# Kernel tuning notes

Hardware: AMD Instinct MI355X
Metric: run time of the kernel (lower is better)

## Reference

```python
import jax, jax.numpy as jnp
import numpy as np

V, E, H, B, S = 32000, 512, 1024, 128, 64
EPS = 0.05


def setup_inputs() -> dict:
    key = jax.random.key(0)
    ks = jax.random.split(key, 4)
    s = 0.02
    return {
        "emb": jax.random.normal(ks[0], (V, E), jnp.float32) * s,
        "w_ih": jax.random.normal(ks[1], (3 * H, E), jnp.float32) * s,
        "w_hh": jax.random.normal(ks[2], (3 * H, H), jnp.float32) * s,
        "b_ih": jnp.zeros((3 * H,), jnp.float32),
        "b_hh": jnp.zeros((3 * H,), jnp.float32),
        "w_dist": jax.random.normal(ks[3], (V, H), jnp.float32) * s,
        "b_dist": jnp.zeros((V,), jnp.float32),
    }


def reference(emb, w_ih, w_hh, b_ih, b_hh, w_dist, b_dist):
    base = jax.random.key(42)
    log_unif = -jnp.log(jnp.float32(V))  # log prob of uniform draw
    rows = jnp.arange(B)

    def step(carry, t):
        h, x = carry
        # PyTorch GRUCell math
        gx = x @ w_ih.T + b_ih            # [B, 3H]
        gh = h @ w_hh.T + b_hh            # [B, 3H]
        xr, xz, xn = jnp.split(gx, 3, axis=1)
        hr, hz, hn = jnp.split(gh, 3, axis=1)
        r = jax.nn.sigmoid(xr + hr)
        z = jax.nn.sigmoid(xz + hz)
        n = jnp.tanh(xn + r * hn)
        h_new = (1.0 - z) * n + z * h     # [B, H]

        dist = jax.nn.log_softmax(h_new @ w_dist.T + b_dist, axis=-1)  # [B, V]
        dist_sg = jax.lax.stop_gradient(dist)  # .detach() in torch

        k = jax.random.fold_in(base, t)
        k1, k2 = jax.random.split(k)
        # epsilon-exploration: replace whole row by uniform log-prob
        draw = jax.random.uniform(k1, (B,)) <= EPS
        dist_new = jnp.where(draw[:, None], log_unif, dist_sg)
        # Gumbel-max categorical sampling: argmax(dist_new - log(-log U))
        gumbel = -jnp.log(-jnp.log(jax.random.uniform(k2, (B, V))))
        sampled = jnp.argmax(dist_new + gumbel, axis=1)  # [B] int

        logprob = dist[rows, sampled]                                # [B]
        onp = jnp.clip(jnp.exp(dist_sg[rows, sampled]), 1e-8, 1.0)
        offp = jnp.clip(jnp.exp(dist_new[rows, sampled]), 1e-8, 1.0)
        correction = onp / offp
        prob_mean = jnp.mean(jnp.exp(dist_sg), axis=0)               # [V]

        x_next = emb[sampled]  # feed sampled token back in
        return (h_new, x_next), (sampled, correction, logprob, prob_mean)

    h0 = jnp.zeros((B, H), emb.dtype)
    x0 = jnp.broadcast_to(emb[0], (B, E))  # embedding of zero_input
    _, (samp, corr, lp, probs) = jax.lax.scan(step, (h0, x0), jnp.arange(S))
    # stack along time then transpose to [B, S] like torch.cat(..., 1)
    return samp.T, corr.T, lp.T, probs
```

## Files before the change

### kernel.cpp

```cpp
#include <hip/hip_runtime.h>
#include <cstdint>
#include <cmath>

#define V 32000
#define E 512
#define H 1024
#define B 128
#define S 64
#define NCHUNK 8
#define CHUNK 4000
#define PSTRIDE 250
#define BS (B*S)
#define NEG_HUGE (-3.0e38f)

typedef __attribute__((ext_vector_type(8))) short short8;
typedef __attribute__((ext_vector_type(4))) float f32x4;

#define TFR(x0, x1, r) { x0 += x1; x1 = ((x1) << (r)) | ((x1) >> (32 - (r))); x1 ^= x0; }

__host__ __device__ inline void tf2x32(uint32_t k0, uint32_t k1, uint32_t &x0, uint32_t &x1) {
  uint32_t ks2 = k0 ^ k1 ^ 0x1BD11BDAu;
  x0 += k0; x1 += k1;
  TFR(x0,x1,13) TFR(x0,x1,15) TFR(x0,x1,26) TFR(x0,x1,6)
  x0 += k1;  x1 += ks2 + 1u;
  TFR(x0,x1,17) TFR(x0,x1,29) TFR(x0,x1,16) TFR(x0,x1,24)
  x0 += ks2; x1 += k0 + 2u;
  TFR(x0,x1,13) TFR(x0,x1,15) TFR(x0,x1,26) TFR(x0,x1,6)
  x0 += k0;  x1 += k1 + 3u;
  TFR(x0,x1,17) TFR(x0,x1,29) TFR(x0,x1,16) TFR(x0,x1,24)
  x0 += k1;  x1 += ks2 + 4u;
  TFR(x0,x1,13) TFR(x0,x1,15) TFR(x0,x1,26) TFR(x0,x1,6)
  x0 += ks2; x1 += k0 + 5u;
}

__device__ __forceinline__ uint32_t tf_bits32(uint32_t ka, uint32_t kb, uint32_t idx) {
  uint32_t x0 = 0u, x1 = idx;
  tf2x32(ka, kb, x0, x1);
  return x0 ^ x1;
}

__device__ __forceinline__ float bits_to_unif(uint32_t b) {
  return __uint_as_float((b >> 9) | 0x3f800000u) - 1.0f;
}

__device__ __forceinline__ float sigmoidf_(float x) { return 1.0f / (1.0f + expf(-x)); }

__device__ __forceinline__ ushort f2bf(float f) {
  uint32_t u = __float_as_uint(f);
  uint32_t r = u + 0x7FFFu + ((u >> 16) & 1u);
  return (ushort)(r >> 16);
}
__device__ __forceinline__ float bf2f(ushort h) { return __uint_as_float(((uint32_t)h) << 16); }

__device__ __forceinline__ void gload16(const ushort* g, ushort* l) {
  __builtin_amdgcn_global_load_lds((const __attribute__((address_space(1))) void*)g,
                                   (__attribute__((address_space(3))) void*)l, 16, 0, 0);
}

template<int BM, int BN, int BK, int TM, int TN>
__device__ void gemm_tile(const float* __restrict__ A, const float* __restrict__ Wt,
                          const float* __restrict__ bias, float* __restrict__ C,
                          int N, int K, int mblk, int nblk)
{
  constexpr int WP = BN + 4;
  __shared__ __align__(16) float As[BK][BM];
  __shared__ __align__(16) float Ws[BK][WP];
  const int tid = threadIdx.x;
  constexpr int TX = BN / TN;
  constexpr int TY = BM / TM;
  static_assert(TX * TY == 256, "bad tiling");
  const int tx = tid % TX, ty = tid / TX;
  const int n0 = tx * TN, m0 = ty * TM;

  float acc[TM][TN];
#pragma unroll
  for (int i = 0; i < TM; ++i)
#pragma unroll
    for (int j = 0; j < TN; ++j) acc[i][j] = 0.0f;

  constexpr int NA = (BM * BK / 4) / 256;
  constexpr int NW = (BN * BK / 4) / 256;
  static_assert(NA >= 1 && NW >= 1, "tile too small");

  for (int k0 = 0; k0 < K; k0 += BK) {
    __syncthreads();
#pragma unroll
    for (int q = 0; q < NA; ++q) {
      int idx = q * 256 + tid;
      int m = idx / (BK / 4), c = idx % (BK / 4);
      float4 v = *(const float4*)&A[(size_t)(mblk + m) * K + k0 + 4 * c];
      As[4*c+0][m] = v.x; As[4*c+1][m] = v.y; As[4*c+2][m] = v.z; As[4*c+3][m] = v.w;
    }
#pragma unroll
    for (int q = 0; q < NW; ++q) {
      int idx = q * 256 + tid;
      int n = idx / (BK / 4), c = idx % (BK / 4);
      float4 v = *(const float4*)&Wt[(size_t)(nblk + n) * K + k0 + 4 * c];
      Ws[4*c+0][n] = v.x; Ws[4*c+1][n] = v.y; Ws[4*c+2][n] = v.z; Ws[4*c+3][n] = v.w;
    }
    __syncthreads();
#pragma unroll
    for (int k = 0; k < BK; ++k) {
      float a[TM], w[TN];
#pragma unroll
      for (int i = 0; i < TM; ++i) a[i] = As[k][m0 + i];
#pragma unroll
      for (int j = 0; j < TN; ++j) w[j] = Ws[k][n0 + j];
#pragma unroll
      for (int i = 0; i < TM; ++i)
#pragma unroll
        for (int j = 0; j < TN; ++j) acc[i][j] += a[i] * w[j];
    }
  }
#pragma unroll
  for (int i = 0; i < TM; ++i)
#pragma unroll
    for (int j = 0; j < TN; ++j)
      C[(size_t)(mblk + m0 + i) * N + nblk + n0 + j] = acc[i][j] + bias[nblk + n0 + j];
}

__global__ __launch_bounds__(256) void gemm_dist_k(const float* __restrict__ h,
    const float* __restrict__ w_dist, const float* __restrict__ b_dist,
    float* __restrict__ logits)
{
  gemm_tile<128, 64, 16, 8, 4>(h, w_dist, b_dist, logits, V, H, 0, blockIdx.x * 64);
}

__global__ __launch_bounds__(256) void gemm_gru_k(const float* __restrict__ x,
    const float* __restrict__ h, const float* __restrict__ w_ih, const float* __restrict__ w_hh,
    const float* __restrict__ b_ih, const float* __restrict__ b_hh,
    float* __restrict__ gx, float* __restrict__ gh)
{
  int b = blockIdx.x;
  if (b < 96) {
    int rb = b & 1, cb = b >> 1;
    gemm_tile<64, 64, 16, 4, 4>(x, w_ih, b_ih, gx, 3 * H, E, rb * 64, cb * 64);
  } else {
    b -= 96;
    int rb = b & 1, cb = b >> 1;
    gemm_tile<64, 64, 16, 4, 4>(h, w_hh, b_hh, gh, 3 * H, H, rb * 64, cb * 64);
  }
}

__global__ __launch_bounds__(256) void wsplit_k(const float* __restrict__ w,
    ushort* __restrict__ whi, ushort* __restrict__ wlo, int n4)
{
  int idx = blockIdx.x * 256 + threadIdx.x;
  if (idx >= n4) return;
  size_t i = (size_t)idx * 4;
  float4 v = *(const float4*)&w[i];
  ushort h0 = f2bf(v.x), h1 = f2bf(v.y), h2 = f2bf(v.z), h3 = f2bf(v.w);
  ushort l0 = f2bf(v.x - bf2f(h0)), l1 = f2bf(v.y - bf2f(h1));
  ushort l2 = f2bf(v.z - bf2f(h2)), l3 = f2bf(v.w - bf2f(h3));
  ushort4 hv = {h0, h1, h2, h3}, lv = {l0, l1, l2, l3};
  *(ushort4*)&whi[i] = hv;
  *(ushort4*)&wlo[i] = lv;
}

__global__ __launch_bounds__(256) void gru_gates_k(const float* __restrict__ gx,
    const float* __restrict__ gh, float* __restrict__ h,
    ushort* __restrict__ hhi, ushort* __restrict__ hlo)
{
  int idx = blockIdx.x * 256 + threadIdx.x;
  int b = idx >> 10, j = idx & 1023;
  const float* gxb = gx + (size_t)b * 3 * H;
  const float* ghb = gh + (size_t)b * 3 * H;
  float r = sigmoidf_(gxb[j] + ghb[j]);
  float z = sigmoidf_(gxb[H + j] + ghb[H + j]);
  float n = tanhf(gxb[2 * H + j] + r * ghb[2 * H + j]);
  float hn = (1.0f - z) * n + z * h[idx];
  h[idx] = hn;
  ushort hi = f2bf(hn);
  hhi[idx] = hi;
  hlo[idx] = f2bf(hn - bf2f(hi));
}

__global__ __launch_bounds__(512) void gemm_dist_mfma(const ushort* __restrict__ hhi,
    const ushort* __restrict__ hlo, const ushort* __restrict__ whi,
    const ushort* __restrict__ wlo, const float* __restrict__ b_dist,
    float* __restrict__ logits,
    float* __restrict__ pm, float* __restrict__ ps,
    float* __restrict__ pbest, int* __restrict__ pidx,
    uint32_t k1a, uint32_t k1b, uint32_t k2a, uint32_t k2b)
{
  __shared__ ushort Ah[2][128 * 32], Al[2][128 * 32], Wh[2][128 * 32], Wl[2][128 * 32];
  __shared__ float rm[2 * 128], rs[2 * 128], rb_[2 * 128];
  __shared__ int   ri[2 * 128];
  __shared__ uint32_t sdraw[128];
  const int tid = threadIdx.x;
  const int wave = tid >> 6, lane = tid & 63;
  const int wm = (wave & 3) * 32;
  const int wn = (wave >> 2) * 64;
  const int nblk = blockIdx.x * 128;
  const int l15 = lane & 15;
  const int q = lane >> 4;

  if (tid < 128)
    sdraw[tid] = (bits_to_unif(tf_bits32(k1a, k1b, (uint32_t)tid)) <= 0.05f) ? 1u : 0u;

  const int sr = tid >> 2;
  const int gq8 = ((tid & 3) ^ ((sr >> 1) & 3)) * 8;
  const size_t arow = (size_t)sr * 1024 + gq8;
  const size_t wrow = (size_t)(nblk + sr) * 1024 + gq8;
  const int wbase = wave * 512;

#define DIST_STAGE(bf, kk) {                                   \
    gload16(&hhi[arow + (kk)], &Ah[bf][wbase]);                \
    gload16(&hlo[arow + (kk)], &Al[bf][wbase]);                \
    gload16(&whi[wrow + (kk)], &Wh[bf][wbase]);                \
    gload16(&wlo[wrow + (kk)], &Wl[bf][wbase]);                \
  }

  f32x4 acc[2][4] = {};

  DIST_STAGE(0, 0);

  int buf = 0;
  for (int k0 = 0; k0 < 1024; k0 += 32, buf ^= 1) {
    const bool more = (k0 + 32 < 1024);
    if (more) {
      DIST_STAGE(buf ^ 1, k0 + 32);
      asm volatile("s_waitcnt vmcnt(4)" ::: "memory");
    } else {
      asm volatile("s_waitcnt vmcnt(0)" ::: "memory");
    }
    __builtin_amdgcn_sched_barrier(0);
    __builtin_amdgcn_s_barrier();
    __builtin_amdgcn_sched_barrier(0);

    short8 ah[2], al[2], wh[4], wl[4];
#pragma unroll
    for (int mt = 0; mt < 2; ++mt) {
      int row = wm + mt * 16 + l15;
      int off = row * 32 + ((q ^ ((row >> 1) & 3)) * 8);
      ah[mt] = *(const short8*)&Ah[buf][off];
      al[mt] = *(const short8*)&Al[buf][off];
    }
#pragma unroll
    for (int nt = 0; nt < 4; ++nt) {
      int row = wn + nt * 16 + l15;
      int off = row * 32 + ((q ^ ((row >> 1) & 3)) * 8);
      wh[nt] = *(const short8*)&Wh[buf][off];
      wl[nt] = *(const short8*)&Wl[buf][off];
    }
#pragma unroll
    for (int mt = 0; mt < 2; ++mt)
#pragma unroll
      for (int nt = 0; nt < 4; ++nt) {
        acc[mt][nt] = __builtin_amdgcn_mfma_f32_16x16x32_bf16(ah[mt], wh[nt], acc[mt][nt], 0, 0, 0);
        acc[mt][nt] = __builtin_amdgcn_mfma_f32_16x16x32_bf16(al[mt], wh[nt], acc[mt][nt], 0, 0, 0);
        acc[mt][nt] = __builtin_amdgcn_mfma_f32_16x16x32_bf16(ah[mt], wl[nt], acc[mt][nt], 0, 0, 0);
      }

    __builtin_amdgcn_s_barrier();
  }
#undef DIST_STAGE

  float bv[4];
#pragma unroll
  for (int nt = 0; nt < 4; ++nt) bv[nt] = b_dist[nblk + wn + nt * 16 + l15];

  const float LOGU = -logf((float)V);
#pragma unroll
  for (int mt = 0; mt < 2; ++mt) {
#pragma unroll
    for (int reg = 0; reg < 4; ++reg) {
      const int r = wm + mt * 16 + q * 4 + reg;
      const bool draw = sdraw[r] != 0u;
      float m0 = NEG_HUGE, s0 = 0.0f, best = NEG_HUGE;
      int bi = 2147483647;
#pragma unroll
      for (int nt = 0; nt < 4; ++nt) {
        const int col = nblk + wn + nt * 16 + l15;
        float a = acc[mt][nt][reg] + bv[nt];
        logits[(size_t)r * V + col] = a;
        if (a > m0) { s0 = s0 * expf(m0 - a) + 1.0f; m0 = a; } else { s0 += expf(a - m0); }
        uint32_t bits = tf_bits32(k2a, k2b, (uint32_t)(r * V + col));
        float g = -logf(-logf(bits_to_unif(bits)));
        float key = draw ? (LOGU + g) : (a + g);
        if (key > best) { best = key; bi = col; }
      }
#pragma unroll
      for (int off = 1; off < 16; off <<= 1) {
        float mo = __shfl_xor(m0, off);
        float so = __shfl_xor(s0, off);
        float M = fmaxf(m0, mo);
        s0 = s0 * expf(m0 - M) + so * expf(mo - M);
        m0 = M;
        float bo = __shfl_xor(best, off);
        int io = __shfl_xor(bi, off);
        if (bo > best || (bo == best && io < bi)) { best = bo; bi = io; }
      }
      if (l15 == 0) {
        const int slot = (wave >> 2) * 128 + r;
        rm[slot] = m0; rs[slot] = s0; rb_[slot] = best; ri[slot] = bi;
      }
    }
  }
  __syncthreads();
  if (tid < 128) {
    float ma = rm[tid], sa = rs[tid], mb = rm[128 + tid], sb = rs[128 + tid];
    float M = fmaxf(ma, mb);
    float s = sa * expf(ma - M) + sb * expf(mb - M);
    pm[tid * PSTRIDE + blockIdx.x] = M;
    ps[tid * PSTRIDE + blockIdx.x] = s;
    float va = rb_[tid], vb = rb_[128 + tid];
    int ia = ri[tid], ib = ri[128 + tid];
    if (vb > va || (vb == va && ib < ia)) { va = vb; ia = ib; }
    pbest[tid * PSTRIDE + blockIdx.x] = va;
    pidx[tid * PSTRIDE + blockIdx.x] = ia;
  }
}

__device__ void gemm64_bf16x3(const ushort* __restrict__ Ahi_g, const ushort* __restrict__ Alo_g,
    const ushort* __restrict__ Whi_g, const ushort* __restrict__ Wlo_g,
    const float* __restrict__ bias, float* __restrict__ C,
    int N, int K, int mblk, int nblk)
{
  __shared__ ushort Ah[2][64 * 32], Al[2][64 * 32], Wh[2][64 * 32], Wl[2][64 * 32];
  const int tid = threadIdx.x;
  const int wave = tid >> 6, lane = tid & 63;
  const int wm = (wave & 1) * 32, wn = (wave >> 1) * 32;
  const int l15 = lane & 15, q = lane >> 4;

  const int sr = tid >> 2;
  const int gq8 = ((tid & 3) ^ ((sr >> 1) & 3)) * 8;
  const size_t arow = (size_t)(mblk + sr) * K + gq8;
  const size_t wrow = (size_t)(nblk + sr) * K + gq8;
  const int wbase = wave * 512;

#define GRU_STAGE(bf, kk) {                                    \
    gload16(&Ahi_g[arow + (kk)], &Ah[bf][wbase]);              \
    gload16(&Alo_g[arow + (kk)], &Al[bf][wbase]);              \
    gload16(&Whi_g[wrow + (kk)], &Wh[bf][wbase]);              \
    gload16(&Wlo_g[wrow + (kk)], &Wl[bf][wbase]);              \
  }

  f32x4 acc[2][2] = {};

  GRU_STAGE(0, 0);

  int buf = 0;
  for (int k0 = 0; k0 < K; k0 += 32, buf ^= 1) {
    const bool more = (k0 + 32 < K);
    if (more) {
      GRU_STAGE(buf ^ 1, k0 + 32);
      asm volatile("s_waitcnt vmcnt(4)" ::: "memory");
    } else {
      asm volatile("s_waitcnt vmcnt(0)" ::: "memory");
    }
    __builtin_amdgcn_sched_barrier(0);
    __builtin_amdgcn_s_barrier();
    __builtin_amdgcn_sched_barrier(0);

    short8 ah[2], al[2], wh[2], wl[2];
#pragma unroll
    for (int mt = 0; mt < 2; ++mt) {
      int row = wm + mt * 16 + l15;
      int off = row * 32 + ((q ^ ((row >> 1) & 3)) * 8);
      ah[mt] = *(const short8*)&Ah[buf][off];
      al[mt] = *(const short8*)&Al[buf][off];
    }
#pragma unroll
    for (int nt = 0; nt < 2; ++nt) {
      int row = wn + nt * 16 + l15;
      int off = row * 32 + ((q ^ ((row >> 1) & 3)) * 8);
      wh[nt] = *(const short8*)&Wh[buf][off];
      wl[nt] = *(const short8*)&Wl[buf][off];
    }
#pragma unroll
    for (int mt = 0; mt < 2; ++mt)
#pragma unroll
      for (int nt = 0; nt < 2; ++nt) {
        acc[mt][nt] = __builtin_amdgcn_mfma_f32_16x16x32_bf16(ah[mt], wh[nt], acc[mt][nt], 0, 0, 0);
        acc[mt][nt] = __builtin_amdgcn_mfma_f32_16x16x32_bf16(al[mt], wh[nt], acc[mt][nt], 0, 0, 0);
        acc[mt][nt] = __builtin_amdgcn_mfma_f32_16x16x32_bf16(ah[mt], wl[nt], acc[mt][nt], 0, 0, 0);
      }

    __builtin_amdgcn_s_barrier();
  }
#undef GRU_STAGE

#pragma unroll
  for (int nt = 0; nt < 2; ++nt) {
    int col = nblk + wn + nt * 16 + l15;
    float bv = bias[col];
#pragma unroll
    for (int mt = 0; mt < 2; ++mt) {
      int rbase = mblk + wm + mt * 16 + (lane >> 4) * 4;
#pragma unroll
      for (int reg = 0; reg < 4; ++reg)
        C[(size_t)(rbase + reg) * N + col] = acc[mt][nt][reg] + bv;
    }
  }
}

__global__ __launch_bounds__(256) void gemm_gru_mfma(
    const ushort* __restrict__ xhi, const ushort* __restrict__ xlo,
    const ushort* __restrict__ hhi, const ushort* __restrict__ hlo,
    const ushort* __restrict__ wihhi, const ushort* __restrict__ wihlo,
    const ushort* __restrict__ whhhi, const ushort* __restrict__ whhlo,
    const float* __restrict__ b_ih, const float* __restrict__ b_hh,
    float* __restrict__ gx, float* __restrict__ gh)
{
  int b = blockIdx.x;
  if (b < 96) {
    int mblk = (b & 1) * 64, nblk = (b >> 1) * 64;
    gemm64_bf16x3(xhi, xlo, wihhi, wihlo, b_ih, gx, 3 * H, E, mblk, nblk);
  } else {
    b -= 96;
    int mblk = (b & 1) * 64, nblk = (b >> 1) * 64;
    gemm64_bf16x3(hhi, hlo, whhhi, whhlo, b_hh, gh, 3 * H, H, mblk, nblk);
  }
}

__global__ __launch_bounds__(256) void init_k(const float* __restrict__ emb,
    float* __restrict__ h, float* __restrict__ x,
    ushort* __restrict__ hhi, ushort* __restrict__ hlo,
    ushort* __restrict__ xhi, ushort* __restrict__ xlo)
{
  int i = blockIdx.x * 256 + threadIdx.x;
  if (i < B * H) { h[i] = 0.0f; hhi[i] = 0; hlo[i] = 0; }
  if (i < B * E) {
    float v = emb[i & (E - 1)];
    x[i] = v;
    ushort hi = f2bf(v);
    xhi[i] = hi;
    xlo[i] = f2bf(v - bf2f(hi));
  }
}

__global__ __launch_bounds__(256) void sample_partial_k(const float* __restrict__ logits,
    float* __restrict__ pm, float* __restrict__ ps,
    float* __restrict__ pbest, int* __restrict__ pidx,
    uint32_t k1a, uint32_t k1b, uint32_t k2a, uint32_t k2b)
{
  const int b = blockIdx.x & 127, chunk = blockIdx.x >> 7;
  const int tid = threadIdx.x;
  const bool draw = bits_to_unif(tf_bits32(k1a, k1b, (uint32_t)b)) <= 0.05f;
  const float LOGU = -logf((float)V);
  const int vbeg = chunk * CHUNK, vend = vbeg + CHUNK;
  float m0 = -INFINITY, s0 = 0.0f, best = -INFINITY;
  int bi = 2147483647;
  for (int v = vbeg + tid; v < vend; v += 256) {
    float a = logits[(size_t)b * V + v];
    if (a > m0) { s0 = s0 * expf(m0 - a) + 1.0f; m0 = a; } else { s0 += expf(a - m0); }
    uint32_t bits = tf_bits32(k2a, k2b, (uint32_t)(b * V + v));
    float g = -logf(-logf(bits_to_unif(bits)));
    float key = draw ? (LOGU + g) : (a + g);
    if (key > best) { best = key; bi = v; }
  }
  __shared__ float shm[256], shs[256], sv[256];
  __shared__ int si[256];
  shm[tid] = m0; shs[tid] = s0; sv[tid] = best; si[tid] = bi;
  __syncthreads();
  for (int off = 128; off > 0; off >>= 1) {
    if (tid < off) {
      float ma = shm[tid], sa = shs[tid];
      float mb = shm[tid + off], sb = shs[tid + off];
      float M = fmaxf(ma, mb);
      shm[tid] = M;
      shs[tid] = sa * expf(ma - M) + sb * expf(mb - M);
      float va = sv[tid], vb = sv[tid + off];
      int ia = si[tid], ib = si[tid + off];
      if (vb > va || (vb == va && ib < ia)) { sv[tid] = vb; si[tid] = ib; }
    }
    __syncthreads();
  }
  if (tid == 0) {
    pm[b * PSTRIDE + chunk] = shm[0]; ps[b * PSTRIDE + chunk] = shs[0];
    pbest[b * PSTRIDE + chunk] = sv[0]; pidx[b * PSTRIDE + chunk] = si[0];
  }
}

__global__ __launch_bounds__(128) void sample_final_gather_k(const float* __restrict__ logits,
    const float* __restrict__ pm, const float* __restrict__ ps,
    const float* __restrict__ pbest, const int* __restrict__ pidx,
    float* __restrict__ rowm, float* __restrict__ rowz, int* __restrict__ samp,
    const float* __restrict__ emb, float* __restrict__ x,
    ushort* __restrict__ xhi, ushort* __restrict__ xlo,
    float* __restrict__ out, int t, uint32_t k1a, uint32_t k1b, int nchunk)
{
  __shared__ float shm[128], shs[128], shb[128];
  __shared__ int shi[128];
  __shared__ int sh_idx;
  const int b = blockIdx.x, tid = threadIdx.x;
  float m0 = NEG_HUGE, s0 = 0.0f, best = NEG_HUGE;
  int bi = 2147483647;
  for (int c = tid; c < nchunk; c += 128) {
    float ma = pm[b * PSTRIDE + c], sa = ps[b * PSTRIDE + c];
    float M = fmaxf(m0, ma);
    s0 = s0 * expf(m0 - M) + sa * expf(ma - M);
    m0 = M;
    float v = pbest[b * PSTRIDE + c];
    int ix = pidx[b * PSTRIDE + c];
    if (v > best || (v == best && ix < bi)) { best = v; bi = ix; }
  }
  shm[tid] = m0; shs[tid] = s0; shb[tid] = best; shi[tid] = bi;
  __syncthreads();
  for (int off = 64; off > 0; off >>= 1) {
    if (tid < off) {
      float ma = shm[tid], sa = shs[tid];
      float mb = shm[tid + off], sb = shs[tid + off];
      float M = fmaxf(ma, mb);
      shm[tid] = M;
      shs[tid] = sa * expf(ma - M) + sb * expf(mb - M);
      float va = shb[tid], vb = shb[tid + off];
      int ia = shi[tid], ib = shi[tid + off];
      if (vb > va || (vb == va && ib < ia)) { shb[tid] = vb; shi[tid] = ib; }
    }
    __syncthreads();
  }
  if (tid == 0) {
    float mrow = shm[0];
    float z0 = logf(shs[0]);
    int idx = shi[0];
    rowm[b] = mrow; rowz[b] = z0;
    float lp = (logits[(size_t)b * V + idx] - mrow) - z0;
    bool draw = bits_to_unif(tf_bits32(k1a, k1b, (uint32_t)b)) <= 0.05f;
    float corr = 1.0f;
    if (draw) {
      const float LOGU = -logf((float)V);
      float onp = fminf(fmaxf(expf(lp), 1e-8f), 1.0f);
      float offp = fminf(fmaxf(expf(LOGU), 1e-8f), 1.0f);
      corr = onp / offp;
    }
    out[b * S + t] = (float)idx;
    out[BS + b * S + t] = corr;
    out[2 * BS + b * S + t] = lp;
    samp[b] = idx;
    sh_idx = idx;
  }
  __syncthreads();
  const int row = sh_idx;
  float4 v = *(const float4*)&emb[(size_t)row * E + tid * 4];
  *(float4*)&x[(size_t)b * E + tid * 4] = v;
  ushort h0 = f2bf(v.x), h1 = f2bf(v.y), h2 = f2bf(v.z), h3 = f2bf(v.w);
  ushort l0 = f2bf(v.x - bf2f(h0)), l1 = f2bf(v.y - bf2f(h1));
  ushort l2 = f2bf(v.z - bf2f(h2)), l3 = f2bf(v.w - bf2f(h3));
  ushort4 hv = {h0, h1, h2, h3}, lv = {l0, l1, l2, l3};
  *(ushort4*)&xhi[(size_t)b * E + tid * 4] = hv;
  *(ushort4*)&xlo[(size_t)b * E + tid * 4] = lv;
}

__global__ __launch_bounds__(256) void probs_k(const float* __restrict__ logits,
    const float* __restrict__ rowm, const float* __restrict__ rowz,
    float* __restrict__ out, int t)
{
  __shared__ float sm[B], sz[B];
  __shared__ float red[256];
  const int tid = threadIdx.x;
  if (tid < B) { sm[tid] = rowm[tid]; sz[tid] = rowz[tid]; }
  __syncthreads();
  const int v = blockIdx.x * 64 + (tid & 63);
  const int bh = tid >> 6;
  float acc = 0.0f;
#pragma unroll 4
  for (int i = 0; i < 32; ++i) {
    int b = bh * 32 + i;
    acc += expf((logits[(size_t)b * V + v] - sm[b]) - sz[b]);
  }
  red[tid] = acc;
  __syncthreads();
  if (tid < 64) {
    float r = red[tid] + red[tid + 64] + red[tid + 128] + red[tid + 192];
    out[3 * BS + (size_t)t * V + v] = r * (1.0f / 128.0f);
  }
}

extern "C" void kernel_launch(void* const* d_in, const int* in_sizes, int n_in,
                              void* d_out, int out_size, void* d_ws, size_t ws_size,
                              hipStream_t stream) {
  (void)in_sizes; (void)n_in; (void)out_size;
  const float* emb    = (const float*)d_in[0];
  const float* w_ih   = (const float*)d_in[1];
  const float* w_hh   = (const float*)d_in[2];
  const float* b_ih   = (const float*)d_in[3];
  const float* b_hh   = (const float*)d_in[4];
  const float* w_dist = (const float*)d_in[5];
  const float* b_dist = (const float*)d_in[6];
  float* out = (float*)d_out;

  float* ws = (float*)d_ws;
  float* h      = ws;
  float* x      = h + B * H;
  float* gx     = x + B * E;
  float* gh     = gx + B * 3 * H;
  float* logits = gh + B * 3 * H;
  float* pm     = logits + (size_t)B * V;
  float* ps     = pm + B * PSTRIDE;
  float* pbest  = ps + B * PSTRIDE;
  int*   pidx   = (int*)(pbest + B * PSTRIDE);
  float* rowm   = (float*)(pidx + B * PSTRIDE);
  float* rowz   = rowm + B;
  int*   samp   = (int*)(rowz + B);
  ushort* hhi   = (ushort*)(samp + B);
  ushort* hlo   = hhi + (size_t)B * H;
  ushort* whi   = hlo + (size_t)B * H;
  ushort* wlo   = whi + (size_t)V * H;
  ushort* xhi   = wlo + (size_t)V * H;
  ushort* xlo   = xhi + (size_t)B * E;
  ushort* wihhi = xlo + (size_t)B * E;
  ushort* wihlo = wihhi + (size_t)3 * H * E;
  ushort* whhhi = wihlo + (size_t)3 * H * E;
  ushort* whhlo = whhhi + (size_t)3 * H * H;

  size_t need_dist = (size_t)((char*)xhi - (char*)d_ws);
  size_t need_gru  = (size_t)((char*)(whhlo + (size_t)3 * H * H) - (char*)d_ws);
  const bool use_dist_mfma = ws_size >= need_dist;
  const bool use_gru_mfma  = ws_size >= need_gru;

  init_k<<<512, 256, 0, stream>>>(emb, h, x, hhi, hlo, xhi, xlo);
  if (use_dist_mfma)
    wsplit_k<<<(V * H / 4 + 255) / 256, 256, 0, stream>>>(w_dist, whi, wlo, V * H / 4);
  if (use_gru_mfma) {
    wsplit_k<<<(3 * H * E / 4 + 255) / 256, 256, 0, stream>>>(w_ih, wihhi, wihlo, 3 * H * E / 4);
    wsplit_k<<<(3 * H * H / 4 + 255) / 256, 256, 0, stream>>>(w_hh, whhhi, whhlo, 3 * H * H / 4);
  }

  const uint32_t base0 = 0u, base1 = 42u;
  for (int t = 0; t < S; ++t) {
    uint32_t f0 = 0u, f1 = (uint32_t)t;
    tf2x32(base0, base1, f0, f1);
    uint32_t k1a = 0u, k1b = 0u; tf2x32(f0, f1, k1a, k1b);
    uint32_t k2a = 0u, k2b = 1u; tf2x32(f0, f1, k2a, k2b);

    if (use_gru_mfma)
      gemm_gru_mfma<<<192, 256, 0, stream>>>(xhi, xlo, hhi, hlo, wihhi, wihlo,
                                             whhhi, whhlo, b_ih, b_hh, gx, gh);
    else
      gemm_gru_k<<<192, 256, 0, stream>>>(x, h, w_ih, w_hh, b_ih, b_hh, gx, gh);
    gru_gates_k<<<512, 256, 0, stream>>>(gx, gh, h, hhi, hlo);
    int nchunk;
    if (use_dist_mfma) {
      gemm_dist_mfma<<<250, 512, 0, stream>>>(hhi, hlo, whi, wlo, b_dist, logits,
                                              pm, ps, pbest, pidx, k1a, k1b, k2a, k2b);
      nchunk = 250;
    } else {
      gemm_dist_k<<<500, 256, 0, stream>>>(h, w_dist, b_dist, logits);
      sample_partial_k<<<1024, 256, 0, stream>>>(logits, pm, ps, pbest, pidx,
                                                 k1a, k1b, k2a, k2b);
      nchunk = NCHUNK;
    }
    sample_final_gather_k<<<128, 128, 0, stream>>>(logits, pm, ps, pbest, pidx,
                                                   rowm, rowz, samp, emb, x, xhi, xlo,
                                                   out, t, k1a, k1b, nchunk);
    probs_k<<<500, 256, 0, stream>>>(logits, rowm, rowz, out, t);
  }
}
```

Measured before the change: 6.269 ms.

## Fuse GRU GEMMs with gate math and overlap prior-step probs in one kernel

Adds a fused kernel that computes both GRU input and hidden GEMMs per 16-column gate slice and applies the gate nonlinearity in registers, removing the gx/gh round-trip and the separate gates launch. Extra blocks in the same launch compute the previous step's probability mean, so probs_k is deferred by one step, and the hidden state is double-buffered to allow this. It also changes the pipelining of the old GRU GEMM to wait fully each iteration. The fused kernel waits on all loads every k-step, which reduces load/compute overlap.

```diff
diff --git a/kernel.cpp b/kernel.cpp
--- a/kernel.cpp
+++ b/kernel.cpp
@@ -173,6 +173,160 @@
   ushort hi = f2bf(hn);
   hhi[idx] = hi;
   hlo[idx] = f2bf(hn - bf2f(hi));
+}
+
+__global__ __launch_bounds__(256) void gru_fused_k(
+    const ushort* __restrict__ xhi, const ushort* __restrict__ xlo,
+    const ushort* __restrict__ hhi_r, const ushort* __restrict__ hlo_r,
+    const float* __restrict__ h_r,
+    const ushort* __restrict__ wihhi, const ushort* __restrict__ wihlo,
+    const ushort* __restrict__ whhhi, const ushort* __restrict__ whhlo,
+    const float* __restrict__ b_ih, const float* __restrict__ b_hh,
+    float* __restrict__ h_w, ushort* __restrict__ hhi_w, ushort* __restrict__ hlo_w,
+    const float* __restrict__ logits, const float* __restrict__ rowm,
+    const float* __restrict__ rowz, float* __restrict__ out, int t)
+{
+  if (blockIdx.x >= 128) {
+    if (t == 0) return;
+    __shared__ float sm[B], sz[B];
+    __shared__ float red[256];
+    const int tid = threadIdx.x;
+    if (tid < B) { sm[tid] = rowm[tid]; sz[tid] = rowz[tid]; }
+    __syncthreads();
+    const int pb = blockIdx.x - 128;
+    const int v = pb * 64 + (tid & 63);
+    const int bh = tid >> 6;
+    float acc = 0.0f;
+#pragma unroll 4
+    for (int i = 0; i < 32; ++i) {
+      int bb = bh * 32 + i;
+      acc += expf((logits[(size_t)bb * V + v] - sm[bb]) - sz[bb]);
+    }
+    red[tid] = acc;
+    __syncthreads();
+    if (tid < 64) {
+      float r = red[tid] + red[tid + 64] + red[tid + 128] + red[tid + 192];
+      out[3 * BS + (size_t)(t - 1) * V + v] = r * (1.0f / 128.0f);
+    }
+    return;
+  }
+
+  __shared__ ushort Ah[2][64 * 32], Al[2][64 * 32];
+  __shared__ ushort Wh3[2][48 * 32], Wl3[2][48 * 32];
+  const int tid = threadIdx.x;
+  const int wave = tid >> 6, lane = tid & 63;
+  const int l15 = lane & 15, q = lane >> 4;
+  const int blk = blockIdx.x;
+  const int mblk = (blk & 1) * 64;
+  const int jb = (blk >> 1) * 16;
+
+  const int atr = wave * 16 + (lane >> 2);
+  const int sq8 = ((lane & 3) ^ ((lane >> 3) & 3)) * 8;
+  const int wgr = jb + (lane >> 2);
+  const int aBase = wave * 512;
+  const int wBase = wave * 512;
+
+  f32x4 accX[3] = {}, accH[3] = {};
+
+  {
+    const size_t aRow = (size_t)(mblk + atr) * E + sq8;
+    const size_t wRow = (size_t)(wave * H + wgr) * E + sq8;
+#define STAGE1(bf, kk) {                                           \
+      gload16(&xhi[aRow + (kk)], &Ah[bf][aBase]);                  \
+      gload16(&xlo[aRow + (kk)], &Al[bf][aBase]);                  \
+      if (wave < 3) {                                              \
+        gload16(&wihhi[wRow + (kk)], &Wh3[bf][wBase]);             \
+        gload16(&wihlo[wRow + (kk)], &Wl3[bf][wBase]);             \
+      } }
+    STAGE1(0, 0);
+    asm volatile("s_waitcnt vmcnt(0)" ::: "memory");
+    __builtin_amdgcn_sched_barrier(0);
+    __builtin_amdgcn_s_barrier();
+    int buf = 0;
+    for (int k0 = 0; k0 < E; k0 += 32, buf ^= 1) {
+      if (k0 + 32 < E) STAGE1(buf ^ 1, k0 + 32);
+      const int ar = wave * 16 + l15;
+      const int aoff = ar * 32 + ((q ^ ((ar >> 1) & 3)) * 8);
+      short8 ah = *(const short8*)&Ah[buf][aoff];
+      short8 al = *(const short8*)&Al[buf][aoff];
+#pragma unroll
+      for (int g = 0; g < 3; ++g) {
+        const int wr = g * 16 + l15;
+        const int woff = wr * 32 + ((q ^ ((wr >> 1) & 3)) * 8);
+        short8 wh = *(const short8*)&Wh3[buf][woff];
+        short8 wl = *(const short8*)&Wl3[buf][woff];
+        accX[g] = __builtin_amdgcn_mfma_f32_16x16x32_bf16(ah, wh, accX[g], 0, 0, 0);
+        accX[g] = __builtin_amdgcn_mfma_f32_16x16x32_bf16(al, wh, accX[g], 0, 0, 0);
+        accX[g] = __builtin_amdgcn_mfma_f32_16x16x32_bf16(ah, wl, accX[g], 0, 0, 0);
+      }
+      asm volatile("s_waitcnt vmcnt(0)" ::: "memory");
+      __builtin_amdgcn_sched_barrier(0);
+      __builtin_amdgcn_s_barrier();
+    }
+#undef STAGE1
+  }
+
+  {
+    const size_t aRow = (size_t)(mblk + atr) * H + sq8;
+    const size_t wRow = (size_t)(wave * H + wgr) * H + sq8;
+#define STAGE2(bf, kk) {                                           \
+      gload16(&hhi_r[aRow + (kk)], &Ah[bf][aBase]);                \
+      gload16(&hlo_r[aRow + (kk)], &Al[bf][aBase]);                \
+      if (wave < 3) {                                              \
+        gload16(&whhhi[wRow + (kk)], &Wh3[bf][wBase]);             \
+        gload16(&whhlo[wRow + (kk)], &Wl3[bf][wBase]);             \
+      } }
+    STAGE2(0, 0);
+    asm volatile("s_waitcnt vmcnt(0)" ::: "memory");
+    __builtin_amdgcn_sched_barrier(0);
+    __builtin_amdgcn_s_barrier();
+    int buf = 0;
+    for (int k0 = 0; k0 < H; k0 += 32, buf ^= 1) {
+      if (k0 + 32 < H) STAGE2(buf ^ 1, k0 + 32);
+      const int ar = wave * 16 + l15;
+      const int aoff = ar * 32 + ((q ^ ((ar >> 1) & 3)) * 8);
+      short8 ah = *(const short8*)&Ah[buf][aoff];
+      short8 al = *(const short8*)&Al[buf][aoff];
+#pragma unroll
+      for (int g = 0; g < 3; ++g) {
+        const int wr = g * 16 + l15;
+        const int woff = wr * 32 + ((q ^ ((wr >> 1) & 3)) * 8);
+        short8 wh = *(const short8*)&Wh3[buf][woff];
+        short8 wl = *(const short8*)&Wl3[buf][woff];
+        accH[g] = __builtin_amdgcn_mfma_f32_16x16x32_bf16(ah, wh, accH[g], 0, 0, 0);
+        accH[g] = __builtin_amdgcn_mfma_f32_16x16x32_bf16(al, wh, accH[g], 0, 0, 0);
+        accH[g] = __builtin_amdgcn_mfma_f32_16x16x32_bf16(ah, wl, accH[g], 0, 0, 0);
+      }
+      asm volatile("s_waitcnt vmcnt(0)" ::: "memory");
+      __builtin_amdgcn_sched_barrier(0);
+      __builtin_amdgcn_s_barrier();
+    }
+#undef STAGE2
+  }
+
+  const int colj = jb + l15;
+  float bihv[3], bhhv[3];
+#pragma unroll
+  for (int g = 0; g < 3; ++g) {
+    bihv[g] = b_ih[g * H + colj];
+    bhhv[g] = b_hh[g * H + colj];
+  }
+#pragma unroll
+  for (int reg = 0; reg < 4; ++reg) {
+    const int row = mblk + wave * 16 + q * 4 + reg;
+    const size_t oi = (size_t)row * H + colj;
+    float gxr = accX[0][reg] + bihv[0], ghr = accH[0][reg] + bhhv[0];
+    float gxz = accX[1][reg] + bihv[1], ghz = accH[1][reg] + bhhv[1];
+    float gxn = accX[2][reg] + bihv[2], ghn = accH[2][reg] + bhhv[2];
+    float r = sigmoidf_(gxr + ghr);
+    float z = sigmoidf_(gxz + ghz);
+    float n = tanhf(gxn + r * ghn);
+    float hn = (1.0f - z) * n + z * h_r[oi];
+    h_w[oi] = hn;
+    ushort hi = f2bf(hn);
+    hhi_w[oi] = hi;
+    hlo_w[oi] = f2bf(hn - bf2f(hi));
+  }
 }
 
 __global__ __launch_bounds__(512) void gemm_dist_mfma(const ushort* __restrict__ hhi,
@@ -339,19 +493,13 @@
   f32x4 acc[2][2] = {};
 
   GRU_STAGE(0, 0);
+  asm volatile("s_waitcnt vmcnt(0)" ::: "memory");
+  __builtin_amdgcn_sched_barrier(0);
+  __builtin_amdgcn_s_barrier();
 
   int buf = 0;
   for (int k0 = 0; k0 < K; k0 += 32, buf ^= 1) {
-    const bool more = (k0 + 32 < K);
-    if (more) {
-      GRU_STAGE(buf ^ 1, k0 + 32);
-      asm volatile("s_waitcnt vmcnt(4)" ::: "memory");
-    } else {
-      asm volatile("s_waitcnt vmcnt(0)" ::: "memory");
-    }
-    __builtin_amdgcn_sched_barrier(0);
-    __builtin_amdgcn_s_barrier();
-    __builtin_amdgcn_sched_barrier(0);
+    if (k0 + 32 < K) GRU_STAGE(buf ^ 1, k0 + 32);
 
     short8 ah[2], al[2], wh[2], wl[2];
 #pragma unroll
@@ -377,6 +525,8 @@
         acc[mt][nt] = __builtin_amdgcn_mfma_f32_16x16x32_bf16(ah[mt], wl[nt], acc[mt][nt], 0, 0, 0);
       }
 
+    asm volatile("s_waitcnt vmcnt(0)" ::: "memory");
+    __builtin_amdgcn_sched_barrier(0);
     __builtin_amdgcn_s_barrier();
   }
 #undef GRU_STAGE
@@ -605,10 +755,15 @@
   ushort* whhhi = wihlo + (size_t)3 * H * E;
   ushort* whhlo = whhhi + (size_t)3 * H * H;
 
+  float*  h1   = gx;
+  ushort* hhi1 = (ushort*)(gx + B * H);
+  ushort* hlo1 = hhi1 + (size_t)B * H;
+
   size_t need_dist = (size_t)((char*)xhi - (char*)d_ws);
   size_t need_gru  = (size_t)((char*)(whhlo + (size_t)3 * H * H) - (char*)d_ws);
   const bool use_dist_mfma = ws_size >= need_dist;
   const bool use_gru_mfma  = ws_size >= need_gru;
+  const bool fused = use_dist_mfma && use_gru_mfma;
 
   init_k<<<512, 256, 0, stream>>>(emb, h, x, hhi, hlo, xhi, xlo);
   if (use_dist_mfma)
@@ -618,6 +773,10 @@
     wsplit_k<<<(3 * H * H / 4 + 255) / 256, 256, 0, stream>>>(w_hh, whhhi, whhlo, 3 * H * H / 4);
   }
 
+  float*  hF[2]  = {h, h1};
+  ushort* hHI[2] = {hhi, hhi1};
+  ushort* hLO[2] = {hlo, hlo1};
+
   const uint32_t base0 = 0u, base1 = 42u;
   for (int t = 0; t < S; ++t) {
     uint32_t f0 = 0u, f1 = (uint32_t)t;
@@ -625,26 +784,41 @@
     uint32_t k1a = 0u, k1b = 0u; tf2x32(f0, f1, k1a, k1b);
     uint32_t k2a = 0u, k2b = 1u; tf2x32(f0, f1, k2a, k2b);
 
-    if (use_gru_mfma)
-      gemm_gru_mfma<<<192, 256, 0, stream>>>(xhi, xlo, hhi, hlo, wihhi, wihlo,
-                                             whhhi, whhlo, b_ih, b_hh, gx, gh);
-    else
-      gemm_gru_k<<<192, 256, 0, stream>>>(x, h, w_ih, w_hh, b_ih, b_hh, gx, gh);
-    gru_gates_k<<<512, 256, 0, stream>>>(gx, gh, h, hhi, hlo);
-    int nchunk;
-    if (use_dist_mfma) {
-      gemm_dist_mfma<<<250, 512, 0, stream>>>(hhi, hlo, whi, wlo, b_dist, logits,
+    if (fused) {
+      const int rd = t & 1, wr = rd ^ 1;
+      gru_fused_k<<<628, 256, 0, stream>>>(xhi, xlo, hHI[rd], hLO[rd], hF[rd],
+                                           wihhi, wihlo, whhhi, whhlo, b_ih, b_hh,
+                                           hF[wr], hHI[wr], hLO[wr],
+                                           logits, rowm, rowz, out, t);
+      gemm_dist_mfma<<<250, 512, 0, stream>>>(hHI[wr], hLO[wr], whi, wlo, b_dist, logits,
                                               pm, ps, pbest, pidx, k1a, k1b, k2a, k2b);
-      nchunk = 250;
+      sample_final_gather_k<<<128, 128, 0, stream>>>(logits, pm, ps, pbest, pidx,
+                                                     rowm, rowz, samp, emb, x, xhi, xlo,
+                                                     out, t, k1a, k1b, 250);
     } else {
-      gemm_dist_k<<<500, 256, 0, stream>>>(h, w_dist, b_dist, logits);
-      sample_partial_k<<<1024, 256, 0, stream>>>(logits, pm, ps, pbest, pidx,
-                                                 k1a, k1b, k2a, k2b);
-      nchunk = NCHUNK;
-    }
-    sample_final_gather_k<<<128, 128, 0, stream>>>(logits, pm, ps, pbest, pidx,
-                                                   rowm, rowz, samp, emb, x, xhi, xlo,
-                                                   out, t, k1a, k1b, nchunk);
-    probs_k<<<500, 256, 0, stream>>>(logits, rowm, rowz, out, t);
-  }
-}
+      if (use_gru_mfma)
+        gemm_gru_mfma<<<192, 256, 0, stream>>>(xhi, xlo, hhi, hlo, wihhi, wihlo,
+                                               whhhi, whhlo, b_ih, b_hh, gx, gh);
+      else
+        gemm_gru_k<<<192, 256, 0, stream>>>(x, h, w_ih, w_hh, b_ih, b_hh, gx, gh);
+      gru_gates_k<<<512, 256, 0, stream>>>(gx, gh, h, hhi, hlo);
+      int nchunk;
+      if (use_dist_mfma) {
+        gemm_dist_mfma<<<250, 512, 0, stream>>>(hhi, hlo, whi, wlo, b_dist, logits,
+                                                pm, ps, pbest, pidx, k1a, k1b, k2a, k2b);
+        nchunk = 250;
+      } else {
+        gemm_dist_k<<<500, 256, 0, stream>>>(h, w_dist, b_dist, logits);
+        sample_partial_k<<<1024, 256, 0, stream>>>(logits, pm, ps, pbest, pidx,
+                                                   k1a, k1b, k2a, k2b);
+        nchunk = NCHUNK;
+      }
+      sample_final_gather_k<<<128, 128, 0, stream>>>(logits, pm, ps, pbest, pidx,
+                                                     rowm, rowz, samp, emb, x, xhi, xlo,
+                                                     out, t, k1a, k1b, nchunk);
+      probs_k<<<500, 256, 0, stream>>>(logits, rowm, rowz, out, t);
+    }
+  }
+  if (fused)
+    probs_k<<<500, 256, 0, stream>>>(logits, rowm, rowz, out, S - 1);
+}
```

Result: faster. 6.054 ms (-3.4%).
